# Performance work log

Measured on AMD Instinct MI355X. Metric: run time of the kernel, lower is better.

The kernel has to match this reference:

```python
import jax, jax.numpy as jnp
import numpy as np

USER_NUM = 50000
ITEM_NUM = 100000
N = USER_NUM + ITEM_NUM
D = 64
NUM_LAYERS = 3          # len(hidden_units) in config
MAIN_LAYERS = NUM_LAYERS + 1  # forward() loops over hidden_units AFTER prepending embedding_dim
LMBD = 1e-4
SSL_TAU = 0.5
SSL_WEIGHT = 0.1
E = 2_000_000
E_KEEP = 1_800_000
EPS = 1e-12


def _edge_weights(src, dst, n):
    # calculate_graph: norm = out_degree^-0.5, edge_weight = norm[src]*norm[dst]
    deg = jnp.zeros((n,), jnp.float32).at[src].add(1.0)
    norm = jnp.power(jnp.maximum(deg, 1.0), -0.5)
    return norm[src] * norm[dst]


def setup_inputs() -> dict:
    key = jax.random.key(0)
    ks = jax.random.split(key, 12)
    user_emb = jax.random.normal(ks[0], (USER_NUM, D), jnp.float32) * 0.1
    item_emb = jax.random.normal(ks[1], (ITEM_NUM, D), jnp.float32) * 0.1
    src = jax.random.randint(ks[2], (E,), 0, N)
    dst = jax.random.randint(ks[3], (E,), 0, N)
    w = _edge_weights(src, dst, N)
    # augmented graphs (ED): random edge subset + self loops
    self_loop = jnp.arange(N, dtype=src.dtype)
    src1 = jnp.concatenate([jax.random.randint(ks[4], (E_KEEP - N,), 0, N) if E_KEEP - N > 0 else src[:0], jax.random.randint(ks[4], (E_KEEP - N,), 0, N)[:0], self_loop])
    src1 = jnp.concatenate([jax.random.randint(ks[4], (E_KEEP,), 0, N), self_loop])
    dst1 = jnp.concatenate([jax.random.randint(ks[5], (E_KEEP,), 0, N), self_loop])
    src1 = src1[: E_KEEP + N - 0]
    w1 = _edge_weights(src1, dst1, N)
    src2 = jnp.concatenate([jax.random.randint(ks[6], (E_KEEP,), 0, N), self_loop])
    dst2 = jnp.concatenate([jax.random.randint(ks[7], (E_KEEP,), 0, N), self_loop])
    w2 = _edge_weights(src2, dst2, N)
    user_id = jax.random.randint(ks[8], (4096,), 0, USER_NUM)
    item_id = jax.random.randint(ks[9], (4096,), 0, ITEM_NUM)
    neg_item_id = jax.random.randint(ks[10], (4096,), 0, ITEM_NUM)
    return {"user_emb": user_emb, "item_emb": item_emb, "src": src, "dst": dst, "w": w,
            "src1": src1, "dst1": dst1, "w1": w1, "src2": src2, "dst2": dst2, "w2": w2,
            "user_id": user_id, "item_id": item_id, "neg_item_id": neg_item_id}


def _l2norm(x):
    n = jnp.linalg.norm(x, axis=1, keepdims=True)
    return x / jnp.maximum(n, EPS)


def _propagate(user_emb, item_emb, src, dst, w, layers):
    # LightGCNConv per layer: m = h[src]*w; h' = scatter-sum to dst; L2 normalize
    u_list, i_list = [user_emb], [item_emb]
    u, i = user_emb, item_emb
    for _ in range(layers):
        h = jnp.concatenate([u, i], axis=0)            # [N, D]
        m = h[src] * w[:, None]                        # [E, D]
        h = jax.ops.segment_sum(m, dst, num_segments=N)
        h = _l2norm(h)
        u, i = h[:USER_NUM], h[USER_NUM:]
        u_list.append(u)
        i_list.append(i)
    fu = jnp.mean(jnp.stack(u_list, axis=1), axis=1)
    fi = jnp.mean(jnp.stack(i_list, axis=1), axis=1)
    return fu, fi


def reference(user_emb, item_emb, src, dst, w, src1, dst1, w1, src2, dst2, w2, user_id, item_id, neg_item_id):
    # main propagation (note: MAIN_LAYERS = NUM_LAYERS+1, faithful to the source bug)
    fu, fi = _propagate(user_emb, item_emb, src, dst, w, MAIN_LAYERS)
    ue = fu[user_id]
    pe = fi[item_id]
    ne = fi[neg_item_id]
    # BPR loss
    pos = jnp.sum(ue * pe, axis=1)
    neg = jnp.sum(ue * ne, axis=1)
    bpr = -jnp.mean(jax.nn.log_sigmoid(pos - neg))
    reg = (jnp.sum(ue ** 2) + jnp.sum(pe ** 2) + jnp.sum(ne ** 2)) / 2.0
    bpr_loss = bpr + LMBD * reg / ue.shape[0]
    # SSL loss on two augmented views (NUM_LAYERS layers each)
    u1, i1 = _propagate(user_emb, item_emb, src1, dst1, w1, NUM_LAYERS)
    u2, i2 = _propagate(user_emb, item_emb, src2, dst2, w2, NUM_LAYERS)
    ue1 = _l2norm(u1[user_id]); ue2 = _l2norm(u2[user_id]); au2 = _l2norm(u2)
    v1 = jnp.exp(jnp.sum(ue1 * ue2, axis=1) / SSL_TAU)
    v2 = jnp.sum(jnp.exp(ue1 @ au2.T / SSL_TAU), axis=1)
    ssl_user = -jnp.sum(jnp.log(v1 / v2))
    ie1 = _l2norm(i1[item_id]); ie2 = _l2norm(i2[item_id]); ai2 = _l2norm(i2)
    v3 = jnp.exp(jnp.sum(ie1 * ie2, axis=1) / SSL_TAU)
    v4 = jnp.sum(jnp.exp(ie1 @ ai2.T / SSL_TAU), axis=1)
    ssl_item = -jnp.sum(jnp.log(v3 / v4))
    ssl_loss = (ssl_item + ssl_user) * SSL_WEIGHT
    return bpr_loss + ssl_loss
```

## Files before the change

kernel.cpp:

```cpp
#include <hip/hip_runtime.h>
#include <math.h>
#include <stdint.h>

#define USER_NUM 50000
#define ITEM_NUM 100000
#define NN (USER_NUM + ITEM_NUM)
#define D 64
#define TAU_INV 2.0f
#define LMBD 0.0001f
#define NCITER 16
#define NRG 64
#define NBLK ((NN + 255) / 256)

typedef __bf16 bf16x8 __attribute__((ext_vector_type(8)));
typedef float  f32x4  __attribute__((ext_vector_type(4)));

static __device__ __forceinline__ unsigned short f2bf(float x) {
    union { float f; unsigned u; } v; v.f = x;
    unsigned r = v.u + 0x7FFFu + ((v.u >> 16) & 1u);
    return (unsigned short)(r >> 16);
}
static __device__ __forceinline__ float bf2f(unsigned short b) {
    union { unsigned u; float f; } v; v.u = ((unsigned)b) << 16;
    return v.f;
}

__global__ void init_kernel(const float* __restrict__ ue, const float* __restrict__ ie,
                            unsigned short* __restrict__ hb, float* __restrict__ acc) {
    int i = blockIdx.x * 256 + threadIdx.x;
    if (i < NN * D) {
        float v = (i < USER_NUM * D) ? ue[i] : ie[i - USER_NUM * D];
        hb[i] = f2bf(v); acc[i] = v;
    }
}

__global__ void deg_kernel(const int* __restrict__ dst, int* __restrict__ deg, int E) {
    int i = blockIdx.x * 256 + threadIdx.x;
    if (i < E) atomicAdd(&deg[dst[i]], 1);
}

__global__ void scan_reduce_kernel(const int* __restrict__ deg, int* __restrict__ bsum) {
    __shared__ int sd[256];
    int tid = threadIdx.x;
    int i = blockIdx.x * 256 + tid;
    sd[tid] = (i < NN) ? deg[i] : 0;
    __syncthreads();
    for (int o = 128; o; o >>= 1) { if (tid < o) sd[tid] += sd[tid + o]; __syncthreads(); }
    if (tid == 0) bsum[blockIdx.x] = sd[0];
}

__global__ void scan_mid_kernel(int* __restrict__ bsum, int* __restrict__ rowptr, int nblk) {
    __shared__ int sd[1024];
    int tid = threadIdx.x;
    int v = (tid < nblk) ? bsum[tid] : 0;
    sd[tid] = v;
    __syncthreads();
    for (int o = 1; o < 1024; o <<= 1) {
        int t = (tid >= o) ? sd[tid - o] : 0;
        __syncthreads();
        sd[tid] += t;
        __syncthreads();
    }
    if (tid < nblk) bsum[tid] = sd[tid] - v;
    if (tid == 0) rowptr[NN] = sd[1023];
}

__global__ void scan_final_kernel(const int* __restrict__ deg, const int* __restrict__ bsum,
                                  int* __restrict__ rowptr, int* __restrict__ cursor) {
    __shared__ int sd[256];
    int tid = threadIdx.x;
    int i = blockIdx.x * 256 + tid;
    int v = (i < NN) ? deg[i] : 0;
    sd[tid] = v;
    __syncthreads();
    for (int o = 1; o < 256; o <<= 1) {
        int t = (tid >= o) ? sd[tid - o] : 0;
        __syncthreads();
        sd[tid] += t;
        __syncthreads();
    }
    if (i < NN) {
        int ex = sd[tid] - v + bsum[blockIdx.x];
        rowptr[i] = ex;
        cursor[i] = ex;
    }
}

__global__ void fill_kernel(const int* __restrict__ src, const int* __restrict__ dst,
                            const float* __restrict__ w, int* __restrict__ cursor,
                            int2* __restrict__ perm, int E) {
    int i = blockIdx.x * 256 + threadIdx.x;
    if (i < E) {
        int p = atomicAdd(&cursor[dst[i]], 1);
        perm[p] = make_int2(src[i], __float_as_int(w[i]));
    }
}

__global__ __launch_bounds__(256) void gather_norm_kernel(const unsigned short* __restrict__ hb,
        const int* __restrict__ rowptr, const int2* __restrict__ perm,
        unsigned short* __restrict__ hn, float* __restrict__ acc) {
    int gid = blockIdx.x * 256 + threadIdx.x;
    int row = gid >> 6;
    int lane = gid & 63;
    if (row >= NN) return;
    int beg = rowptr[row];
    int end = rowptr[row + 1];
    float s = 0.f;
    int e = beg;
    for (; e + 2 <= end; e += 2) {
        int2 p0 = perm[e];
        int2 p1 = perm[e + 1];
        float v0 = bf2f(hb[(size_t)p0.x * D + lane]);
        float v1 = bf2f(hb[(size_t)p1.x * D + lane]);
        s += v0 * __int_as_float(p0.y);
        s += v1 * __int_as_float(p1.y);
    }
    if (e < end) {
        int2 p0 = perm[e];
        s += bf2f(hb[(size_t)p0.x * D + lane]) * __int_as_float(p0.y);
    }
    float q = s * s;
    #pragma unroll
    for (int o = 32; o; o >>= 1) q += __shfl_xor(q, o);
    float y = s / fmaxf(sqrtf(q), 1e-12f);
    size_t idx = (size_t)row * D + lane;
    hn[idx] = f2bf(y);
    acc[idx] += y;
}

__global__ void norm_rows_bf_kernel(float* __restrict__ h, unsigned short* __restrict__ hb) {
    int gid = blockIdx.x * 256 + threadIdx.x;
    int row = gid >> 6;
    int lane = gid & 63;
    if (row >= NN) return;
    size_t idx = (size_t)row * D + lane;
    float x = h[idx];
    float s = x * x;
    #pragma unroll
    for (int o = 32; o; o >>= 1) s += __shfl_xor(s, o);
    float y = x / fmaxf(sqrtf(s), 1e-12f);
    h[idx] = y;
    hb[idx] = f2bf(y);
}

__global__ void bpr_kernel(const float* __restrict__ acc, const int* __restrict__ uid,
                           const int* __restrict__ iid, const int* __restrict__ nid,
                           float* __restrict__ scal, int B) {
    int gid = blockIdx.x * 256 + threadIdx.x;
    int r = gid >> 6;
    int lane = gid & 63;
    if (r >= B) return;
    const float inv = 1.0f / 5.0f;
    float ue = acc[(size_t)uid[r] * D + lane] * inv;
    float pe = acc[(size_t)(USER_NUM + iid[r]) * D + lane] * inv;
    float ne = acc[(size_t)(USER_NUM + nid[r]) * D + lane] * inv;
    float pos = ue * pe, neg = ue * ne, reg = ue * ue + pe * pe + ne * ne;
    #pragma unroll
    for (int o = 32; o; o >>= 1) {
        pos += __shfl_xor(pos, o);
        neg += __shfl_xor(neg, o);
        reg += __shfl_xor(reg, o);
    }
    if (lane == 0) {
        float x = pos - neg;
        float ls = (x >= 0.f) ? (-log1pf(expf(-x))) : (x - log1pf(expf(x)));
        atomicAdd(&scal[0], -ls);
        atomicAdd(&scal[1], reg * 0.5f);
    }
}

__global__ void extract_norm_kernel(const float* __restrict__ acc, const int* __restrict__ uid,
                                    const int* __restrict__ iid, unsigned short* __restrict__ ue1b,
                                    unsigned short* __restrict__ ie1b, int B) {
    int gid = blockIdx.x * 256 + threadIdx.x;
    int t = gid >> 6;
    int lane = gid & 63;
    if (t >= 2 * B) return;
    bool user = (t < B);
    int r = user ? t : (t - B);
    size_t srow = user ? (size_t)uid[r] * D : (size_t)(USER_NUM + iid[r]) * D;
    float x = acc[srow + lane];
    float s = x * x;
    #pragma unroll
    for (int o = 32; o; o >>= 1) s += __shfl_xor(s, o);
    float y = x / fmaxf(sqrtf(s), 1e-12f);
    (user ? ue1b : ie1b)[(size_t)r * D + lane] = f2bf(y);
}

__global__ __launch_bounds__(256) void ssl_mfma_kernel(const unsigned short* __restrict__ Ab,
                                                       const unsigned short* __restrict__ Bb,
                                                       float* __restrict__ rowsum,
                                                       int M, int nc) {
    int bid = blockIdx.x;
    int xcd = bid & 7;
    int inner = bid >> 3;
    int rg = inner & (NRG - 1);
    int cgrp = inner >> 6;
    int colChunk = cgrp * 8 + xcd;
    if (colChunk >= nc) return;

    int wave = threadIdx.x >> 6;
    int lane = threadIdx.x & 63;
    int l15 = lane & 15;
    int lg  = lane >> 4;
    int rgbase = rg * 64;
    int chunkbase = colChunk * (128 * NCITER);

    bf16x8 afr[4][2];
    {
        const unsigned short* ab = Ab + (size_t)(rgbase + l15) * D + lg * 8;
        #pragma unroll
        for (int i = 0; i < 4; i++) {
            afr[i][0] = *(const bf16x8*)(ab + (size_t)i * 16 * D);
            afr[i][1] = *(const bf16x8*)(ab + (size_t)i * 16 * D + 32);
        }
    }

    float rowacc[4][4];
    #pragma unroll
    for (int i = 0; i < 4; i++)
        #pragma unroll
        for (int r = 0; r < 4; r++) rowacc[i][r] = 0.f;

    for (int it = 0; it < NCITER; it++) {
        int cb = chunkbase + it * 128 + wave * 32;
        bf16x8 bfr[2][2];
        bool val[2];
        #pragma unroll
        for (int cf = 0; cf < 2; cf++) {
            int col = cb + cf * 16 + l15;
            val[cf] = (col < M);
            int cc = val[cf] ? col : (M - 1);
            const unsigned short* bp = Bb + (size_t)cc * D + lg * 8;
            bfr[cf][0] = *(const bf16x8*)(bp);
            bfr[cf][1] = *(const bf16x8*)(bp + 32);
        }

        f32x4 acc[4][2];
        #pragma unroll
        for (int i = 0; i < 4; i++)
            #pragma unroll
            for (int cf = 0; cf < 2; cf++)
                acc[i][cf] = (f32x4){0.f, 0.f, 0.f, 0.f};

        #pragma unroll
        for (int i = 0; i < 4; i++) {
            #pragma unroll
            for (int cf = 0; cf < 2; cf++) {
                acc[i][cf] = __builtin_amdgcn_mfma_f32_16x16x32_bf16(afr[i][0], bfr[cf][0], acc[i][cf], 0, 0, 0);
                acc[i][cf] = __builtin_amdgcn_mfma_f32_16x16x32_bf16(afr[i][1], bfr[cf][1], acc[i][cf], 0, 0, 0);
            }
        }

        #pragma unroll
        for (int i = 0; i < 4; i++) {
            #pragma unroll
            for (int r = 0; r < 4; r++) {
                float e0 = val[0] ? __expf(TAU_INV * acc[i][0][r]) : 0.f;
                float e1 = val[1] ? __expf(TAU_INV * acc[i][1][r]) : 0.f;
                rowacc[i][r] += e0 + e1;
            }
        }
    }

    #pragma unroll
    for (int i = 0; i < 4; i++) {
        #pragma unroll
        for (int r = 0; r < 4; r++) {
            float s = rowacc[i][r];
            s += __shfl_xor(s, 1);
            s += __shfl_xor(s, 2);
            s += __shfl_xor(s, 4);
            s += __shfl_xor(s, 8);
            if (l15 == 0) atomicAdd(&rowsum[rgbase + i * 16 + lg * 4 + r], s);
        }
    }
}

__global__ void ssl_fin_kernel(const unsigned short* __restrict__ ue1b,
                               const unsigned short* __restrict__ ie1b,
                               const float* __restrict__ A2, const int* __restrict__ uid,
                               const int* __restrict__ iid, const float* __restrict__ rsU,
                               const float* __restrict__ rsI, float* __restrict__ scal, int B) {
    int gid = blockIdx.x * 256 + threadIdx.x;
    int t = gid >> 6;
    int lane = gid & 63;
    if (t >= 2 * B) return;
    bool user = (t < B);
    int r = user ? t : (t - B);
    const unsigned short* a = (user ? ue1b : ie1b) + (size_t)r * D;
    size_t brow = user ? (size_t)uid[r] * D : (size_t)(USER_NUM + iid[r]) * D;
    float p = bf2f(a[lane]) * A2[brow + lane];
    #pragma unroll
    for (int o = 32; o; o >>= 1) p += __shfl_xor(p, o);
    if (lane == 0) {
        float contrib = logf((user ? rsU : rsI)[r]) - p * TAU_INV;
        atomicAdd(&scal[user ? 2 : 3], contrib);
    }
}

__global__ void final_kernel(const float* __restrict__ scal, float* __restrict__ out, int B) {
    if (threadIdx.x == 0 && blockIdx.x == 0) {
        float invB = 1.0f / (float)B;
        float bpr_loss = scal[0] * invB + LMBD * scal[1] * invB;
        float ssl_loss = (scal[2] + scal[3]) * 0.1f;
        out[0] = bpr_loss + ssl_loss;
    }
}

extern "C" void kernel_launch(void* const* d_in, const int* in_sizes, int n_in,
                              void* d_out, int out_size, void* d_ws, size_t ws_size,
                              hipStream_t stream) {
    const float* user_emb = (const float*)d_in[0];
    const float* item_emb = (const float*)d_in[1];
    const int*   src  = (const int*)d_in[2];
    const int*   dst  = (const int*)d_in[3];
    const float* w    = (const float*)d_in[4];
    const int*   src1 = (const int*)d_in[5];
    const int*   dst1 = (const int*)d_in[6];
    const float* w1   = (const float*)d_in[7];
    const int*   src2 = (const int*)d_in[8];
    const int*   dst2 = (const int*)d_in[9];
    const float* w2   = (const float*)d_in[10];
    const int* user_id = (const int*)d_in[11];
    const int* item_id = (const int*)d_in[12];
    const int* neg_id  = (const int*)d_in[13];
    int E0 = in_sizes[2];
    int E1 = in_sizes[5];
    int E2 = in_sizes[8];
    int B  = in_sizes[11];

    size_t nd = (size_t)NN * D;
    float* acc = (float*)d_ws;
    unsigned short* hAb = (unsigned short*)(acc + nd);
    unsigned short* hBb = hAb + nd;
    unsigned short* ue1b = hBb + nd;
    unsigned short* ie1b = ue1b + (size_t)B * D;
    float* rsU  = (float*)(ie1b + (size_t)B * D);
    float* rsI  = rsU + B;
    float* scal = rsI + B;
    int* deg    = (int*)(scal + 8);
    int* rowptr = deg + NN;
    int* cursor = rowptr + NN + 1;
    int* bsum   = cursor + NN;
    int2* perm  = (int2*)(((uintptr_t)(bsum + NBLK) + 15) & ~(uintptr_t)15);
    unsigned short* bbuf = hAb;

    hipMemsetAsync(rsU, 0, (size_t)(2 * B + 8) * sizeof(float), stream);

    int gridElem = (NN * D + 255) / 256;
    int gridRows = (NN * 64 + 255) / 256;

    auto propagate = [&](const int* s_, const int* d_, const float* w_, int E_, int layers) {
        hipMemsetAsync(deg, 0, (size_t)NN * sizeof(int), stream);
        int ge = (E_ + 255) / 256;
        deg_kernel<<<ge, 256, 0, stream>>>(d_, deg, E_);
        scan_reduce_kernel<<<NBLK, 256, 0, stream>>>(deg, bsum);
        scan_mid_kernel<<<1, 1024, 0, stream>>>(bsum, rowptr, NBLK);
        scan_final_kernel<<<NBLK, 256, 0, stream>>>(deg, bsum, rowptr, cursor);
        fill_kernel<<<ge, 256, 0, stream>>>(s_, d_, w_, cursor, perm, E_);
        init_kernel<<<gridElem, 256, 0, stream>>>(user_emb, item_emb, hAb, acc);
        unsigned short* cur = hAb;
        unsigned short* nxt = hBb;
        for (int l = 0; l < layers; l++) {
            gather_norm_kernel<<<gridRows, 256, 0, stream>>>(cur, rowptr, perm, nxt, acc);
            unsigned short* t = cur; cur = nxt; nxt = t;
        }
    };

    propagate(src, dst, w, E0, 4);
    bpr_kernel<<<(B * 64) / 256, 256, 0, stream>>>(acc, user_id, item_id, neg_id, scal, B);

    propagate(src1, dst1, w1, E1, 3);
    extract_norm_kernel<<<(2 * B * 64) / 256, 256, 0, stream>>>(acc, user_id, item_id, ue1b, ie1b, B);

    propagate(src2, dst2, w2, E2, 3);
    norm_rows_bf_kernel<<<gridRows, 256, 0, stream>>>(acc, bbuf);

    {
        int ncU = (USER_NUM + 128 * NCITER - 1) / (128 * NCITER);
        int gu = 8 * NRG * ((ncU + 7) / 8);
        ssl_mfma_kernel<<<gu, 256, 0, stream>>>(ue1b, bbuf, rsU, USER_NUM, ncU);
        int ncI = (ITEM_NUM + 128 * NCITER - 1) / (128 * NCITER);
        int gi = 8 * NRG * ((ncI + 7) / 8);
        ssl_mfma_kernel<<<gi, 256, 0, stream>>>(ie1b, bbuf + (size_t)USER_NUM * D, rsI, ITEM_NUM, ncI);
    }

    ssl_fin_kernel<<<(2 * B * 64) / 256, 256, 0, stream>>>(ue1b, ie1b, acc, user_id, item_id,
                                                           rsU, rsI, scal, B);
    final_kernel<<<1, 64, 0, stream>>>(scal, (float*)d_out, B);
}
```

Measured before the change: 2.401 ms.

## Build all three graph CSRs in one batched pass and unroll gather by four

The three graphs' degree counting, prefix scan and CSR fill are merged into single launches over a concatenated 3*NN row space. This replaces three separate build sequences, each with a memset and five kernel launches. The mid-level scan now handles two block sums per thread so it can cover the larger block count. The gather loop is also unrolled from two to four edges per iteration to keep more loads in flight. The cost is a larger workspace for the combined rowptr, cursor and perm arrays, and it relies on the three per-graph row ranges being contiguous in rowptr.

```diff
diff --git a/kernel.cpp b/kernel.cpp
--- a/kernel.cpp
+++ b/kernel.cpp
@@ -10,7 +10,8 @@
 #define LMBD 0.0001f
 #define NCITER 16
 #define NRG 64
-#define NBLK ((NN + 255) / 256)
+#define T3 (3 * NN)
+#define NBLK3 ((T3 + 255) / 256)
 
 typedef __bf16 bf16x8 __attribute__((ext_vector_type(8)));
 typedef float  f32x4  __attribute__((ext_vector_type(4)));
@@ -34,26 +35,34 @@
     }
 }
 
-__global__ void deg_kernel(const int* __restrict__ dst, int* __restrict__ deg, int E) {
+__global__ void deg3_kernel(const int* __restrict__ d0, const int* __restrict__ d1,
+                            const int* __restrict__ d2, int* __restrict__ deg3,
+                            int E0, int E1, int E2) {
     int i = blockIdx.x * 256 + threadIdx.x;
-    if (i < E) atomicAdd(&deg[dst[i]], 1);
+    int d;
+    if (i < E0) d = d0[i];
+    else if (i < E0 + E1) d = NN + d1[i - E0];
+    else if (i < E0 + E1 + E2) d = 2 * NN + d2[i - E0 - E1];
+    else return;
+    atomicAdd(&deg3[d], 1);
 }
 
 __global__ void scan_reduce_kernel(const int* __restrict__ deg, int* __restrict__ bsum) {
     __shared__ int sd[256];
     int tid = threadIdx.x;
     int i = blockIdx.x * 256 + tid;
-    sd[tid] = (i < NN) ? deg[i] : 0;
+    sd[tid] = (i < T3) ? deg[i] : 0;
     __syncthreads();
     for (int o = 128; o; o >>= 1) { if (tid < o) sd[tid] += sd[tid + o]; __syncthreads(); }
     if (tid == 0) bsum[blockIdx.x] = sd[0];
 }
 
-__global__ void scan_mid_kernel(int* __restrict__ bsum, int* __restrict__ rowptr, int nblk) {
+__global__ void scan_mid_kernel(int* __restrict__ bsum, int* __restrict__ totp, int nblk) {
     __shared__ int sd[1024];
     int tid = threadIdx.x;
-    int v = (tid < nblk) ? bsum[tid] : 0;
-    sd[tid] = v;
+    int v0 = (2 * tid < nblk) ? bsum[2 * tid] : 0;
+    int v1 = (2 * tid + 1 < nblk) ? bsum[2 * tid + 1] : 0;
+    sd[tid] = v0 + v1;
     __syncthreads();
     for (int o = 1; o < 1024; o <<= 1) {
         int t = (tid >= o) ? sd[tid - o] : 0;
@@ -61,8 +70,10 @@
         sd[tid] += t;
         __syncthreads();
     }
-    if (tid < nblk) bsum[tid] = sd[tid] - v;
-    if (tid == 0) rowptr[NN] = sd[1023];
+    int base = tid ? sd[tid - 1] : 0;
+    if (2 * tid < nblk) bsum[2 * tid] = base;
+    if (2 * tid + 1 < nblk) bsum[2 * tid + 1] = base + v0;
+    if (tid == 1023) totp[0] = sd[1023];
 }
 
 __global__ void scan_final_kernel(const int* __restrict__ deg, const int* __restrict__ bsum,
@@ -70,7 +81,7 @@
     __shared__ int sd[256];
     int tid = threadIdx.x;
     int i = blockIdx.x * 256 + tid;
-    int v = (i < NN) ? deg[i] : 0;
+    int v = (i < T3) ? deg[i] : 0;
     sd[tid] = v;
     __syncthreads();
     for (int o = 1; o < 256; o <<= 1) {
@@ -79,21 +90,26 @@
         sd[tid] += t;
         __syncthreads();
     }
-    if (i < NN) {
+    if (i < T3) {
         int ex = sd[tid] - v + bsum[blockIdx.x];
         rowptr[i] = ex;
         cursor[i] = ex;
     }
 }
 
-__global__ void fill_kernel(const int* __restrict__ src, const int* __restrict__ dst,
-                            const float* __restrict__ w, int* __restrict__ cursor,
-                            int2* __restrict__ perm, int E) {
+__global__ void fill3_kernel(const int* __restrict__ s0, const int* __restrict__ d0, const float* __restrict__ w0,
+                             const int* __restrict__ s1, const int* __restrict__ d1, const float* __restrict__ w1,
+                             const int* __restrict__ s2, const int* __restrict__ d2, const float* __restrict__ w2,
+                             int* __restrict__ cursor, int2* __restrict__ perm,
+                             int E0, int E1, int E2) {
     int i = blockIdx.x * 256 + threadIdx.x;
-    if (i < E) {
-        int p = atomicAdd(&cursor[dst[i]], 1);
-        perm[p] = make_int2(src[i], __float_as_int(w[i]));
-    }
+    int d, s; float w;
+    if (i < E0) { d = d0[i]; s = s0[i]; w = w0[i]; }
+    else if (i < E0 + E1) { int j = i - E0; d = NN + d1[j]; s = s1[j]; w = w1[j]; }
+    else if (i < E0 + E1 + E2) { int j = i - E0 - E1; d = 2 * NN + d2[j]; s = s2[j]; w = w2[j]; }
+    else return;
+    int p = atomicAdd(&cursor[d], 1);
+    perm[p] = make_int2(s, __float_as_int(w));
 }
 
 __global__ __launch_bounds__(256) void gather_norm_kernel(const unsigned short* __restrict__ hb,
@@ -107,15 +123,19 @@
     int end = rowptr[row + 1];
     float s = 0.f;
     int e = beg;
-    for (; e + 2 <= end; e += 2) {
+    for (; e + 4 <= end; e += 4) {
         int2 p0 = perm[e];
         int2 p1 = perm[e + 1];
+        int2 p2 = perm[e + 2];
+        int2 p3 = perm[e + 3];
         float v0 = bf2f(hb[(size_t)p0.x * D + lane]);
         float v1 = bf2f(hb[(size_t)p1.x * D + lane]);
-        s += v0 * __int_as_float(p0.y);
-        s += v1 * __int_as_float(p1.y);
-    }
-    if (e < end) {
+        float v2 = bf2f(hb[(size_t)p2.x * D + lane]);
+        float v3 = bf2f(hb[(size_t)p3.x * D + lane]);
+        s += v0 * __int_as_float(p0.y) + v1 * __int_as_float(p1.y)
+           + v2 * __int_as_float(p2.y) + v3 * __int_as_float(p3.y);
+    }
+    for (; e < end; e++) {
         int2 p0 = perm[e];
         s += bf2f(hb[(size_t)p0.x * D + lane]) * __int_as_float(p0.y);
     }
@@ -329,6 +349,7 @@
     int E1 = in_sizes[5];
     int E2 = in_sizes[8];
     int B  = in_sizes[11];
+    int ET = E0 + E1 + E2;
 
     size_t nd = (size_t)NN * D;
     float* acc = (float*)d_ws;
@@ -339,42 +360,45 @@
     float* rsU  = (float*)(ie1b + (size_t)B * D);
     float* rsI  = rsU + B;
     float* scal = rsI + B;
-    int* deg    = (int*)(scal + 8);
-    int* rowptr = deg + NN;
-    int* cursor = rowptr + NN + 1;
-    int* bsum   = cursor + NN;
-    int2* perm  = (int2*)(((uintptr_t)(bsum + NBLK) + 15) & ~(uintptr_t)15);
+    int* deg3    = (int*)(scal + 8);
+    int* rowptr3 = deg3 + T3;
+    int* cursor3 = rowptr3 + T3 + 1;
+    int* bsum3   = cursor3 + T3;
+    int2* perm3  = (int2*)(((uintptr_t)(bsum3 + 2048) + 15) & ~(uintptr_t)15);
     unsigned short* bbuf = hAb;
 
     hipMemsetAsync(rsU, 0, (size_t)(2 * B + 8) * sizeof(float), stream);
+    hipMemsetAsync(deg3, 0, (size_t)T3 * sizeof(int), stream);
 
     int gridElem = (NN * D + 255) / 256;
     int gridRows = (NN * 64 + 255) / 256;
-
-    auto propagate = [&](const int* s_, const int* d_, const float* w_, int E_, int layers) {
-        hipMemsetAsync(deg, 0, (size_t)NN * sizeof(int), stream);
-        int ge = (E_ + 255) / 256;
-        deg_kernel<<<ge, 256, 0, stream>>>(d_, deg, E_);
-        scan_reduce_kernel<<<NBLK, 256, 0, stream>>>(deg, bsum);
-        scan_mid_kernel<<<1, 1024, 0, stream>>>(bsum, rowptr, NBLK);
-        scan_final_kernel<<<NBLK, 256, 0, stream>>>(deg, bsum, rowptr, cursor);
-        fill_kernel<<<ge, 256, 0, stream>>>(s_, d_, w_, cursor, perm, E_);
+    int gridE3 = (ET + 255) / 256;
+
+    deg3_kernel<<<gridE3, 256, 0, stream>>>(dst, dst1, dst2, deg3, E0, E1, E2);
+    scan_reduce_kernel<<<NBLK3, 256, 0, stream>>>(deg3, bsum3);
+    scan_mid_kernel<<<1, 1024, 0, stream>>>(bsum3, rowptr3 + T3, NBLK3);
+    scan_final_kernel<<<NBLK3, 256, 0, stream>>>(deg3, bsum3, rowptr3, cursor3);
+    fill3_kernel<<<gridE3, 256, 0, stream>>>(src, dst, w, src1, dst1, w1, src2, dst2, w2,
+                                             cursor3, perm3, E0, E1, E2);
+
+    auto propagate = [&](int g, int layers) {
+        const int* rp = rowptr3 + (size_t)g * NN;
         init_kernel<<<gridElem, 256, 0, stream>>>(user_emb, item_emb, hAb, acc);
         unsigned short* cur = hAb;
         unsigned short* nxt = hBb;
         for (int l = 0; l < layers; l++) {
-            gather_norm_kernel<<<gridRows, 256, 0, stream>>>(cur, rowptr, perm, nxt, acc);
+            gather_norm_kernel<<<gridRows, 256, 0, stream>>>(cur, rp, perm3, nxt, acc);
             unsigned short* t = cur; cur = nxt; nxt = t;
         }
     };
 
-    propagate(src, dst, w, E0, 4);
+    propagate(0, 4);
     bpr_kernel<<<(B * 64) / 256, 256, 0, stream>>>(acc, user_id, item_id, neg_id, scal, B);
 
-    propagate(src1, dst1, w1, E1, 3);
+    propagate(1, 3);
     extract_norm_kernel<<<(2 * B * 64) / 256, 256, 0, stream>>>(acc, user_id, item_id, ue1b, ie1b, B);
 
-    propagate(src2, dst2, w2, E2, 3);
+    propagate(2, 3);
     norm_rows_bf_kernel<<<gridRows, 256, 0, stream>>>(acc, bbuf);
 
     {
```

After: 2.045 ms. 1.17x faster.
